# Optimization experiments

Measured on AMD Instinct MI355X. Metric: run time of the kernel, lower is better.

The kernel has to match this reference:

```python
import jax, jax.numpy as jnp
import numpy as np

B, S, HID, NH = 2, 2048, 1024, 16
HD = HID // NH  # head_dim = 64


def setup_inputs() -> dict:
    key = jax.random.key(0)
    ks = jax.random.split(key, 9)
    init = 0.02
    return {
        "x": jax.random.normal(ks[0], (B, S, HID), dtype=jnp.float32),
        "Wq": jax.random.normal(ks[1], (HID, HID), dtype=jnp.float32) * init,
        "bq": jnp.zeros((HID,), dtype=jnp.float32),
        "Wk": jax.random.normal(ks[2], (HID, HID), dtype=jnp.float32) * init,
        "bk": jnp.zeros((HID,), dtype=jnp.float32),
        "Wv": jax.random.normal(ks[3], (HID, HID), dtype=jnp.float32) * init,
        "bv": jnp.zeros((HID,), dtype=jnp.float32),
        "Wo": jax.random.normal(ks[4], (HID, HID), dtype=jnp.float32) * init,
        "bo": jnp.zeros((HID,), dtype=jnp.float32),
    }


def _split_heads(t):
    # [B, S, HID] -> [B, NH, S, HD]
    return t.reshape(B, S, NH, HD).transpose(0, 2, 1, 3)


def reference(x, Wq, bq, Wk, bk, Wv, bv, Wo, bo):
    q = _split_heads(x @ Wq.T + bq)
    k = _split_heads(x @ Wk.T + bk)
    v = _split_heads(x @ Wv.T + bv)

    # Faithful to source: scores = QK^T / (head_dim ** -0.5) == QK^T * sqrt(head_dim)
    inv_scale = jnp.asarray(HD ** (-0.5), dtype=x.dtype)
    scores = jnp.einsum("bhqd,bhkd->bhqk", q, k) / inv_scale

    causal_mask = jnp.triu(jnp.ones((S, S), dtype=bool), k=1)  # True above diagonal
    scores = jnp.where(causal_mask, jnp.asarray(-jnp.inf, dtype=scores.dtype), scores)
    attn = jax.nn.softmax(scores, axis=-1)  # dropout = identity (eval mode)

    ctx = jnp.einsum("bhqk,bhkd->bhqd", attn, v)
    ctx = ctx.transpose(0, 2, 1, 3).reshape(B, S, HID)
    out = ctx @ Wo.T + bo  # out_layer Linear; dropout = identity
    return out, attn
```

## Files before the change

kernel.cpp:

```cpp
#include <hip/hip_runtime.h>
#include <hip/hip_bf16.h>

#define BB   2
#define SS   2048
#define HID  1024
#define NH   16
#define HD   64
#define NEGS -30000.0f

typedef __bf16 bf16x8 __attribute__((ext_vector_type(8)));
typedef __bf16 bf16x4 __attribute__((ext_vector_type(4)));
typedef float  f32x4  __attribute__((ext_vector_type(4)));

static __device__ __forceinline__ f32x4 mfma_bf16(bf16x8 a, bf16x8 b, f32x4 c) {
    return __builtin_amdgcn_mfma_f32_16x16x32_bf16(a, b, c, 0, 0, 0);
}

static __device__ __forceinline__ void split_bf16(float f, __bf16* hp, __bf16* lp) {
    __bf16 h = (__bf16)f;
    *hp = h;
    *lp = (__bf16)(f - (float)h);
}

static __device__ __forceinline__ float clampf(float v, float lo, float hi) {
    return fminf(fmaxf(v, lo), hi);
}

static __device__ __forceinline__ void gll16(const __bf16* g, __bf16* l) {
    __builtin_amdgcn_global_load_lds((const void*)g, (void*)l, 16, 0, 0);
}

static __device__ __forceinline__ void barrier_lds() {
    asm volatile("s_waitcnt lgkmcnt(0)" ::: "memory");
    __builtin_amdgcn_sched_barrier(0);
    __builtin_amdgcn_s_barrier();
    __builtin_amdgcn_sched_barrier(0);
}

__global__ __launch_bounds__(256) void split_kernel(
    const float* __restrict__ x,
    const float* __restrict__ Wq, const float* __restrict__ Wk,
    const float* __restrict__ Wv, const float* __restrict__ Wo,
    __bf16* __restrict__ xh, __bf16* __restrict__ xl,
    __bf16* __restrict__ wqh, __bf16* __restrict__ wql,
    __bf16* __restrict__ wkh, __bf16* __restrict__ wkl,
    __bf16* __restrict__ wvh, __bf16* __restrict__ woh)
{
    const int which = blockIdx.y;
    const int i4 = blockIdx.x * 256 + threadIdx.x;
    if (which == 0) {
        const float4 v = ((const float4*)x)[i4];
        const float* p = (const float*)&v;
        bf16x4 h4, l4v;
#pragma unroll
        for (int j = 0; j < 4; j++) { __bf16 hh, ll; split_bf16(p[j], &hh, &ll); h4[j] = hh; l4v[j] = ll; }
        *(bf16x4*)&xh[(size_t)i4 * 4] = h4;
        *(bf16x4*)&xl[(size_t)i4 * 4] = l4v;
        return;
    }
    if (i4 >= (HID * HID) / 4) return;
    const float* src = which == 1 ? Wq : which == 2 ? Wk : which == 3 ? Wv : Wo;
    const float sc = (which == 1) ? 8.0f : 1.0f;
    const float4 v = ((const float4*)src)[i4];
    const float* p = (const float*)&v;
    bf16x4 h4, l4v;
#pragma unroll
    for (int j = 0; j < 4; j++) { __bf16 hh, ll; split_bf16(p[j] * sc, &hh, &ll); h4[j] = hh; l4v[j] = ll; }
    if (which == 1)      { *(bf16x4*)&wqh[(size_t)i4 * 4] = h4; *(bf16x4*)&wql[(size_t)i4 * 4] = l4v; }
    else if (which == 2) { *(bf16x4*)&wkh[(size_t)i4 * 4] = h4; *(bf16x4*)&wkl[(size_t)i4 * 4] = l4v; }
    else if (which == 3) { *(bf16x4*)&wvh[(size_t)i4 * 4] = h4; }
    else                 { *(bf16x4*)&woh[(size_t)i4 * 4] = h4; }
}

__global__ __launch_bounds__(256) void qkv_kernel(
    const __bf16* __restrict__ xh, const __bf16* __restrict__ xl,
    const __bf16* __restrict__ wqh, const __bf16* __restrict__ wql,
    const __bf16* __restrict__ wkh, const __bf16* __restrict__ wkl,
    const __bf16* __restrict__ wvh,
    const float* __restrict__ bq, const float* __restrict__ bk, const float* __restrict__ bv,
    __bf16* __restrict__ qh, __bf16* __restrict__ ql,
    __bf16* __restrict__ kh, __bf16* __restrict__ kl,
    __bf16* __restrict__ vt)
{
    __shared__ __align__(16) __bf16 smem[18432];
    __bf16* const Ah = smem;
    __bf16* const Al = smem + 4096;
    __bf16* const Bh = smem + 8192;
    __bf16* const Bl = smem + 12288;

    const int stream = blockIdx.x >> 3, ct = blockIdx.x & 7;
    const int t0 = blockIdx.y * 128, c0 = ct * 128;
    const bool qk = stream < 2;
    const __bf16* const Bhg = stream == 0 ? wqh : stream == 1 ? wkh : wvh;
    const __bf16* const Blg = stream == 0 ? wql : wkl;
    const float* const bias = stream == 0 ? bq : stream == 1 ? bk : bv;
    const float bscale = stream == 0 ? 8.0f : 1.0f;

    const int tid = threadIdx.x, wave = tid >> 6, lane = tid & 63;
    const int l16 = lane & 15, quad = lane >> 4;
    const int wr = wave >> 1, wc = wave & 1;

    const int ar0 = tid >> 2,         as0 = (tid & 3) ^ (ar0 & 3);
    const int ar1 = (256 + tid) >> 2, as1 = ((256 + tid) & 3) ^ (ar1 & 3);
    const size_t aoff0 = (size_t)(t0 + ar0) * HID + as0 * 8;
    const size_t aoff1 = (size_t)(t0 + ar1) * HID + as1 * 8;
    const size_t boff0 = (size_t)(c0 + ar0) * HID + as0 * 8;
    const size_t boff1 = (size_t)(c0 + ar1) * HID + as1 * 8;
    const int ld0 = wave << 9, ld1 = (4 + wave) << 9;

    const f32x4 zero4 = {0.f, 0.f, 0.f, 0.f};
    f32x4 acc[4][4];
#pragma unroll
    for (int i = 0; i < 4; i++)
#pragma unroll
        for (int j = 0; j < 4; j++) acc[i][j] = zero4;

    for (int k0 = 0; k0 < HID; k0 += 32) {
        __syncthreads();
        gll16(xh + aoff0 + k0, Ah + ld0);
        gll16(xh + aoff1 + k0, Ah + ld1);
        gll16(Bhg + boff0 + k0, Bh + ld0);
        gll16(Bhg + boff1 + k0, Bh + ld1);
        if (qk) {
            gll16(xl + aoff0 + k0, Al + ld0);
            gll16(xl + aoff1 + k0, Al + ld1);
            gll16(Blg + boff0 + k0, Bl + ld0);
            gll16(Blg + boff1 + k0, Bl + ld1);
        }
        __syncthreads();

        bf16x8 aH[4], aL[4], bHf[4], bLf[4];
#pragma unroll
        for (int mf = 0; mf < 4; mf++) {
            const int row = wr * 64 + mf * 16 + l16;
            const int off = row * 32 + ((quad ^ (row & 3)) << 3);
            aH[mf] = *(const bf16x8*)(Ah + off);
            if (qk) aL[mf] = *(const bf16x8*)(Al + off);
        }
#pragma unroll
        for (int nf = 0; nf < 4; nf++) {
            const int row = wc * 64 + nf * 16 + l16;
            const int off = row * 32 + ((quad ^ (row & 3)) << 3);
            bHf[nf] = *(const bf16x8*)(Bh + off);
            if (qk) bLf[nf] = *(const bf16x8*)(Bl + off);
        }
#pragma unroll
        for (int mf = 0; mf < 4; mf++)
#pragma unroll
            for (int nf = 0; nf < 4; nf++) {
                acc[mf][nf] = mfma_bf16(aH[mf], bHf[nf], acc[mf][nf]);
                if (qk) {
                    acc[mf][nf] = mfma_bf16(aH[mf], bLf[nf], acc[mf][nf]);
                    acc[mf][nf] = mfma_bf16(aL[mf], bHf[nf], acc[mf][nf]);
                }
            }
    }

    const int bidx = t0 >> 11;
    const int s0 = t0 & (SS - 1);

    if (qk) {
        __bf16* const hi = stream == 0 ? qh : kh;
        __bf16* const lo = stream == 0 ? ql : kl;
#pragma unroll
        for (int nf = 0; nf < 4; nf++) {
            const int dcol = c0 + wc * 64 + nf * 16 + l16;
            const int hh = dcol >> 6, d = dcol & 63;
            const float bv_ = bias[dcol] * bscale;
            const size_t ob = (size_t)(bidx * NH + hh) * SS * HD + d;
#pragma unroll
            for (int mf = 0; mf < 4; mf++)
#pragma unroll
                for (int r = 0; r < 4; r++) {
                    const int srow = s0 + wr * 64 + mf * 16 + quad * 4 + r;
                    const float v = clampf(acc[mf][nf][r] + bv_, -1e4f, 1e4f);
                    __bf16 hv, lv;
                    split_bf16(v, &hv, &lv);
                    hi[ob + (size_t)srow * HD] = hv;
                    lo[ob + (size_t)srow * HD] = lv;
                }
        }
    } else {
        __syncthreads();
        __bf16* const Vts = smem + wave * 4608;
#pragma unroll
        for (int nf = 0; nf < 4; nf++) {
            const int dloc = nf * 16 + l16;
            const float bv_ = bias[c0 + wc * 64 + dloc];
#pragma unroll
            for (int mf = 0; mf < 4; mf++)
#pragma unroll
                for (int r = 0; r < 4; r++)
                    Vts[dloc * 72 + mf * 16 + quad * 4 + r] =
                        (__bf16)clampf(acc[mf][nf][r] + bv_, -1e4f, 1e4f);
        }
        const int hh = (c0 + wc * 64) >> 6;
        const size_t vb = (size_t)(bidx * NH + hh) * HD * SS;
        const int sc0 = s0 + wr * 64;
#pragma unroll
        for (int j = 0; j < 8; j++) {
            const int idx = j * 64 + lane;
            const int d = idx >> 3, c8 = idx & 7;
            *(uint4*)&vt[vb + (size_t)d * SS + sc0 + c8 * 8] =
                *(const uint4*)&Vts[d * 72 + c8 * 8];
        }
    }
}

__global__ __launch_bounds__(256) void attn_kernel(
    const __bf16* __restrict__ qh, const __bf16* __restrict__ ql,
    const __bf16* __restrict__ kh, const __bf16* __restrict__ kl,
    const __bf16* __restrict__ vt,
    float* __restrict__ attn, __bf16* __restrict__ ctx)
{
    __shared__ __align__(16) __bf16 Qhs[64][72], Qls[64][72], Ps[64][72];
    __shared__ __align__(16) __bf16 Kh0[4096], Kl0[4096], Kh1[4096], Kl1[4096];
    __shared__ __align__(16) __bf16 Vt0[4096], Vt1[4096];

    const int bid = blockIdx.x;
    const int bh  = bid >> 5;
    const int qt  = 31 - (bid & 31);
    const int b   = bh >> 4, h = bh & 15;

    const int tid  = threadIdx.x;
    const int wave = tid >> 6, lane = tid & 63;
    const int l16  = lane & 15, quad = lane >> 4;

    const int sr0 = tid >> 3,         ss0 = (tid & 7) ^ (sr0 & 7);
    const int sr1 = (256 + tid) >> 3, ss1 = ((256 + tid) & 7) ^ (sr1 & 7);
    const size_t kq0 = (size_t)sr0 * HD + ss0 * 8;
    const size_t kq1 = (size_t)sr1 * HD + ss1 * 8;
    const size_t vq0 = (size_t)sr0 * SS + ss0 * 8;
    const size_t vq1 = (size_t)sr1 * SS + ss1 * 8;
    const int ld0 = wave << 9, ld1 = (4 + wave) << 9;

    const __bf16* const khp = kh + (size_t)bh * SS * HD;
    const __bf16* const klp = kl + (size_t)bh * SS * HD;
    const __bf16* const vtp = vt + (size_t)bh * HD * SS;

#define STAGE_K(kt_, KH, KL) do {                                   \
        const __bf16* kg_ = khp + (size_t)(kt_) * (64 * HD);        \
        const __bf16* lg_ = klp + (size_t)(kt_) * (64 * HD);        \
        gll16(kg_ + kq0, (KH) + ld0); gll16(kg_ + kq1, (KH) + ld1); \
        gll16(lg_ + kq0, (KL) + ld0); gll16(lg_ + kq1, (KL) + ld1); \
    } while (0)
#define STAGE_V(kt_, VT) do {                                       \
        const __bf16* vg_ = vtp + (size_t)(kt_) * 64;               \
        gll16(vg_ + vq0, (VT) + ld0); gll16(vg_ + vq1, (VT) + ld1); \
    } while (0)

    {
        const size_t base = ((size_t)bh * SS + qt * 64) * HD;
#pragma unroll
        for (int i = 0; i < 2; i++) {
            const int idx = tid + i * 256;
            const int row = idx >> 3, c8 = idx & 7;
            *(uint4*)&Qhs[row][c8 * 8] = *(const uint4*)&qh[base + row * HD + c8 * 8];
            *(uint4*)&Qls[row][c8 * 8] = *(const uint4*)&ql[base + row * HD + c8 * 8];
        }
    }
    STAGE_K(0, Kh0, Kl0);
    __syncthreads();

    bf16x8 aHq[2], aLq[2];
#pragma unroll
    for (int ks = 0; ks < 2; ks++) {
        aHq[ks] = *(const bf16x8*)&Qhs[wave * 16 + l16][ks * 32 + quad * 8];
        aLq[ks] = *(const bf16x8*)&Qls[wave * 16 + l16][ks * 32 + quad * 8];
    }

    float m4[4], l4[4];
#pragma unroll
    for (int r = 0; r < 4; r++) { m4[r] = NEGS; l4[r] = 0.f; }
    const f32x4 zero4 = {0.f, 0.f, 0.f, 0.f};

    for (int kt = 0; kt <= qt; kt++) {
        if (kt) __syncthreads();
        if (kt < qt) {
            if (kt & 1) STAGE_K(kt + 1, Kh0, Kl0);
            else        STAGE_K(kt + 1, Kh1, Kl1);
        }
        const __bf16* const Khc = (kt & 1) ? Kh1 : Kh0;
        const __bf16* const Klc = (kt & 1) ? Kl1 : Kl0;

        f32x4 sacc[4] = {zero4, zero4, zero4, zero4};
#pragma unroll
        for (int ks = 0; ks < 2; ks++)
#pragma unroll
            for (int c = 0; c < 4; c++) {
                const int krow = c * 16 + l16;
                const int ko = krow * 64 + (((ks * 4 + quad) ^ (krow & 7)) << 3);
                const bf16x8 bH = *(const bf16x8*)(Khc + ko);
                const bf16x8 bL = *(const bf16x8*)(Klc + ko);
                sacc[c] = mfma_bf16(aHq[ks], bH, sacc[c]);
                sacc[c] = mfma_bf16(aHq[ks], bL, sacc[c]);
                sacc[c] = mfma_bf16(aLq[ks], bH, sacc[c]);
            }
        if (kt == qt) {
#pragma unroll
            for (int c = 0; c < 4; c++) {
                const int col = c * 16 + l16;
#pragma unroll
                for (int r = 0; r < 4; r++)
                    if (col > wave * 16 + quad * 4 + r) sacc[c][r] = NEGS;
            }
        }
#pragma unroll
        for (int r = 0; r < 4; r++) {
            const float mx = fmaxf(fmaxf(sacc[0][r], sacc[1][r]),
                                   fmaxf(sacc[2][r], sacc[3][r]));
            const float mn = fmaxf(m4[r], mx);
            l4[r] = l4[r] * __expf(m4[r] - mn)
                  + __expf(sacc[0][r] - mn) + __expf(sacc[1][r] - mn)
                  + __expf(sacc[2][r] - mn) + __expf(sacc[3][r] - mn);
            m4[r] = mn;
        }
    }

    float il[4];
#pragma unroll
    for (int r = 0; r < 4; r++) {
#pragma unroll
        for (int off = 1; off < 16; off <<= 1) {
            const float mo  = __shfl_xor(m4[r], off);
            const float lo_ = __shfl_xor(l4[r], off);
            const float mn  = fmaxf(m4[r], mo);
            l4[r] = l4[r] * __expf(m4[r] - mn) + lo_ * __expf(mo - mn);
            m4[r] = mn;
        }
        il[r] = (l4[r] > 0.f) ? (1.0f / l4[r]) : 0.f;
    }

    f32x4 cacc[4] = {zero4, zero4, zero4, zero4};

    __syncthreads();
    STAGE_K(0, Kh0, Kl0);
    STAGE_V(0, Vt0);

    for (int kt = 0; kt <= qt; kt++) {
        __syncthreads();
        if (kt < qt) {
            if (kt & 1) { STAGE_K(kt + 1, Kh0, Kl0); STAGE_V(kt + 1, Vt0); }
            else        { STAGE_K(kt + 1, Kh1, Kl1); STAGE_V(kt + 1, Vt1); }
        }
        const __bf16* const Khc = (kt & 1) ? Kh1 : Kh0;
        const __bf16* const Klc = (kt & 1) ? Kl1 : Kl0;
        const __bf16* const Vtc = (kt & 1) ? Vt1 : Vt0;

        f32x4 sacc[4] = {zero4, zero4, zero4, zero4};
#pragma unroll
        for (int ks = 0; ks < 2; ks++)
#pragma unroll
            for (int c = 0; c < 4; c++) {
                const int krow = c * 16 + l16;
                const int ko = krow * 64 + (((ks * 4 + quad) ^ (krow & 7)) << 3);
                const bf16x8 bH = *(const bf16x8*)(Khc + ko);
                const bf16x8 bL = *(const bf16x8*)(Klc + ko);
                sacc[c] = mfma_bf16(aHq[ks], bH, sacc[c]);
                sacc[c] = mfma_bf16(aHq[ks], bL, sacc[c]);
                sacc[c] = mfma_bf16(aLq[ks], bH, sacc[c]);
            }
        if (kt == qt) {
#pragma unroll
            for (int c = 0; c < 4; c++) {
                const int col = c * 16 + l16;
#pragma unroll
                for (int r = 0; r < 4; r++)
                    if (col > wave * 16 + quad * 4 + r) sacc[c][r] = NEGS;
            }
        }
#pragma unroll
        for (int c = 0; c < 4; c++)
#pragma unroll
            for (int r = 0; r < 4; r++) {
                const float p = clampf(__expf(sacc[c][r] - m4[r]) * il[r], 0.f, 1.f);
                Ps[wave * 16 + quad * 4 + r][c * 16 + l16] = (__bf16)p;
            }
        barrier_lds();

#pragma unroll
        for (int i = 0; i < 2; i++) {
            const int idx = tid + i * 256;
            const int row = idx >> 3, c8 = idx & 7;
            const size_t o = ((size_t)bh * SS + qt * 64 + row) * SS + kt * 64 + c8 * 8;
            __bf16 tmp[8];
            *(uint4*)tmp = *(const uint4*)&Ps[row][c8 * 8];
            float4 f0, f1;
            f0.x = (float)tmp[0]; f0.y = (float)tmp[1];
            f0.z = (float)tmp[2]; f0.w = (float)tmp[3];
            f1.x = (float)tmp[4]; f1.y = (float)tmp[5];
            f1.z = (float)tmp[6]; f1.w = (float)tmp[7];
            *(float4*)&attn[o]     = f0;
            *(float4*)&attn[o + 4] = f1;
        }
#pragma unroll
        for (int ks = 0; ks < 2; ks++) {
            const bf16x8 ap = *(const bf16x8*)&Ps[wave * 16 + l16][ks * 32 + quad * 8];
#pragma unroll
            for (int dt = 0; dt < 4; dt++) {
                const int vrow = dt * 16 + l16;
                const int vo = vrow * 64 + (((ks * 4 + quad) ^ (vrow & 7)) << 3);
                cacc[dt] = mfma_bf16(ap, *(const bf16x8*)(Vtc + vo), cacc[dt]);
            }
        }
    }

    const float4 zf4 = {0.f, 0.f, 0.f, 0.f};
    for (int kt = qt + 1; kt < SS / 64; kt++) {
#pragma unroll
        for (int i = 0; i < 4; i++) {
            const int idx = tid + i * 256;
            const int row = idx >> 4, c4 = idx & 15;
            const size_t o = ((size_t)bh * SS + qt * 64 + row) * SS + kt * 64 + c4 * 4;
            *(float4*)&attn[o] = zf4;
        }
    }

#pragma unroll
    for (int dt = 0; dt < 4; dt++) {
        const int d = dt * 16 + l16;
#pragma unroll
        for (int r = 0; r < 4; r++) {
            const int srow = qt * 64 + wave * 16 + quad * 4 + r;
            ctx[(size_t)(b * SS + srow) * HID + h * 64 + d] =
                (__bf16)clampf(cacc[dt][r], -1e4f, 1e4f);
        }
    }
#undef STAGE_K
#undef STAGE_V
}

__global__ __launch_bounds__(256) void out_kernel(
    const __bf16* __restrict__ ctx, const __bf16* __restrict__ woh,
    const float* __restrict__ bo, float* __restrict__ out)
{
    __shared__ __align__(16) __bf16 As[4096], Bs[4096];

    const int o0 = blockIdx.x * 128;
    const int t0 = blockIdx.y * 128;

    const int tid = threadIdx.x, wave = tid >> 6, lane = tid & 63;
    const int l16 = lane & 15, quad = lane >> 4;
    const int wr = wave >> 1, wc = wave & 1;

    const int ar0 = tid >> 2,         as0 = (tid & 3) ^ (ar0 & 3);
    const int ar1 = (256 + tid) >> 2, as1 = ((256 + tid) & 3) ^ (ar1 & 3);
    const size_t aoff0 = (size_t)(t0 + ar0) * HID + as0 * 8;
    const size_t aoff1 = (size_t)(t0 + ar1) * HID + as1 * 8;
    const size_t boff0 = (size_t)(o0 + ar0) * HID + as0 * 8;
    const size_t boff1 = (size_t)(o0 + ar1) * HID + as1 * 8;
    const int ld0 = wave << 9, ld1 = (4 + wave) << 9;

    const f32x4 zero4 = {0.f, 0.f, 0.f, 0.f};
    f32x4 acc[4][4];
#pragma unroll
    for (int i = 0; i < 4; i++)
#pragma unroll
        for (int j = 0; j < 4; j++) acc[i][j] = zero4;

    for (int k0 = 0; k0 < HID; k0 += 32) {
        __syncthreads();
        gll16(ctx + aoff0 + k0, As + ld0);
        gll16(ctx + aoff1 + k0, As + ld1);
        gll16(woh + boff0 + k0, Bs + ld0);
        gll16(woh + boff1 + k0, Bs + ld1);
        __syncthreads();

        bf16x8 aH[4], bHf[4];
#pragma unroll
        for (int mf = 0; mf < 4; mf++) {
            const int row = wr * 64 + mf * 16 + l16;
            aH[mf] = *(const bf16x8*)(As + row * 32 + ((quad ^ (row & 3)) << 3));
        }
#pragma unroll
        for (int nf = 0; nf < 4; nf++) {
            const int row = wc * 64 + nf * 16 + l16;
            bHf[nf] = *(const bf16x8*)(Bs + row * 32 + ((quad ^ (row & 3)) << 3));
        }
#pragma unroll
        for (int mf = 0; mf < 4; mf++)
#pragma unroll
            for (int nf = 0; nf < 4; nf++)
                acc[mf][nf] = mfma_bf16(aH[mf], bHf[nf], acc[mf][nf]);
    }

#pragma unroll
    for (int nf = 0; nf < 4; nf++) {
        const int dcol = o0 + wc * 64 + nf * 16 + l16;
        const float bias = bo[dcol];
#pragma unroll
        for (int mf = 0; mf < 4; mf++)
#pragma unroll
            for (int r = 0; r < 4; r++) {
                const int t = t0 + wr * 64 + mf * 16 + quad * 4 + r;
                out[(size_t)t * HID + dcol] = clampf(acc[mf][nf][r] + bias, -1e4f, 1e4f);
            }
    }
}

extern "C" void kernel_launch(void* const* d_in, const int* in_sizes, int n_in,
                              void* d_out, int out_size, void* d_ws, size_t ws_size,
                              hipStream_t stream) {
    const float* x  = (const float*)d_in[0];
    const float* Wq = (const float*)d_in[1];
    const float* bq = (const float*)d_in[2];
    const float* Wk = (const float*)d_in[3];
    const float* bk = (const float*)d_in[4];
    const float* Wv = (const float*)d_in[5];
    const float* bv = (const float*)d_in[6];
    const float* Wo = (const float*)d_in[7];
    const float* bo = (const float*)d_in[8];

    float* out  = (float*)d_out;
    float* attn = out + (size_t)BB * SS * HID;

    const size_t NQ = (size_t)BB * NH * SS * HD;
    const size_t NW = (size_t)HID * HID;
    __bf16* ws  = (__bf16*)d_ws;
    __bf16* qh  = ws;
    __bf16* ql  = ws + NQ;
    __bf16* kh  = ws + 2 * NQ;
    __bf16* kl  = ws + 3 * NQ;
    __bf16* vt  = ws + 4 * NQ;
    __bf16* xh  = ws + 5 * NQ;
    __bf16* xl  = ws + 6 * NQ;
    __bf16* wqh = ws + 7 * NQ;
    __bf16* wql = wqh + NW;
    __bf16* wkh = wqh + 2 * NW;
    __bf16* wkl = wqh + 3 * NW;
    __bf16* wvh = wqh + 4 * NW;
    __bf16* woh = wqh + 5 * NW;
    __bf16* ctx = xh;

    split_kernel<<<dim3(4096, 5), 256, 0, stream>>>(x, Wq, Wk, Wv, Wo,
                                                    xh, xl, wqh, wql, wkh, wkl, wvh, woh);
    qkv_kernel<<<dim3(24, 32), 256, 0, stream>>>(xh, xl, wqh, wql, wkh, wkl, wvh,
                                                 bq, bk, bv, qh, ql, kh, kl, vt);
    attn_kernel<<<dim3(1024), 256, 0, stream>>>(qh, ql, kh, kl, vt, attn, ctx);
    out_kernel<<<dim3(8, 32), 256, 0, stream>>>(ctx, woh, bo, out);
}
```

Baseline: 817.8 us.

## Restructure attention into 128-row tiles with paired causal segments and staged stores

The attention kernel now uses 512-thread blocks over 128-query-row tiles. Each block processes two paired tiles (qt and 15-qt) so causal work is balanced across 256 blocks, and blocks are mapped so consecutive ones share the same head for K/V reuse. Q is loaded straight into registers, ctx is staged through LDS for coalesced 16-byte stores, and a dummy LDS pad is added to cap occupancy. The QKV epilogue also stages hi/lo tiles through shared memory so global writes are vectorised instead of scalar. The tradeoffs are fewer blocks in flight and extra LDS passes with barriers.

```diff
diff --git a/kernel.cpp b/kernel.cpp
--- a/kernel.cpp
+++ b/kernel.cpp
@@ -160,25 +160,38 @@
     const int s0 = t0 & (SS - 1);
 
     if (qk) {
-        __bf16* const hi = stream == 0 ? qh : kh;
-        __bf16* const lo = stream == 0 ? ql : kl;
-#pragma unroll
-        for (int nf = 0; nf < 4; nf++) {
-            const int dcol = c0 + wc * 64 + nf * 16 + l16;
-            const int hh = dcol >> 6, d = dcol & 63;
-            const float bv_ = bias[dcol] * bscale;
-            const size_t ob = (size_t)(bidx * NH + hh) * SS * HD + d;
-#pragma unroll
-            for (int mf = 0; mf < 4; mf++)
-#pragma unroll
-                for (int r = 0; r < 4; r++) {
-                    const int srow = s0 + wr * 64 + mf * 16 + quad * 4 + r;
-                    const float v = clampf(acc[mf][nf][r] + bv_, -1e4f, 1e4f);
-                    __bf16 hv, lv;
-                    split_bf16(v, &hv, &lv);
-                    hi[ob + (size_t)srow * HD] = hv;
-                    lo[ob + (size_t)srow * HD] = lv;
-                }
+        __bf16* const Es = smem;
+        __bf16* const hi_arr = stream == 0 ? qh : kh;
+        __bf16* const lo_arr = stream == 0 ? ql : kl;
+#pragma unroll
+        for (int pass = 0; pass < 2; pass++) {
+            __syncthreads();
+#pragma unroll
+            for (int nf = 0; nf < 4; nf++) {
+                const int dcl = wc * 64 + nf * 16 + l16;
+                const float bv_ = bias[c0 + dcl] * bscale;
+#pragma unroll
+                for (int mf = 0; mf < 4; mf++)
+#pragma unroll
+                    for (int r = 0; r < 4; r++) {
+                        const int srl = wr * 64 + mf * 16 + quad * 4 + r;
+                        const float v = clampf(acc[mf][nf][r] + bv_, -1e4f, 1e4f);
+                        __bf16 hv, lv;
+                        split_bf16(v, &hv, &lv);
+                        Es[srl * 132 + dcl] = pass ? lv : hv;
+                    }
+            }
+            __syncthreads();
+            __bf16* const dst = pass ? lo_arr : hi_arr;
+#pragma unroll
+            for (int i = 0; i < 8; i++) {
+                const int idx = tid + i * 256;
+                const int row = idx >> 4, c16 = idx & 15;
+                const int hh = (c0 >> 6) + (c16 >> 3);
+                const int dd = (c16 & 7) * 8;
+                const size_t o = ((size_t)(bidx * NH + hh) * SS + (s0 + row)) * HD + dd;
+                *(uint4*)&dst[o] = *(const uint4*)&Es[row * 132 + c16 * 8];
+            }
         }
     } else {
         __syncthreads();
@@ -207,225 +220,235 @@
     }
 }
 
-__global__ __launch_bounds__(256) void attn_kernel(
+__global__ __launch_bounds__(512) void attn_kernel(
     const __bf16* __restrict__ qh, const __bf16* __restrict__ ql,
     const __bf16* __restrict__ kh, const __bf16* __restrict__ kl,
     const __bf16* __restrict__ vt,
     float* __restrict__ attn, __bf16* __restrict__ ctx)
 {
-    __shared__ __align__(16) __bf16 Qhs[64][72], Qls[64][72], Ps[64][72];
     __shared__ __align__(16) __bf16 Kh0[4096], Kl0[4096], Kh1[4096], Kl1[4096];
     __shared__ __align__(16) __bf16 Vt0[4096], Vt1[4096];
+    __shared__ __align__(16) __bf16 Ps[128][72];
+    __shared__ __align__(16) __bf16 _occ_pad[8192];
 
     const int bid = blockIdx.x;
-    const int bh  = bid >> 5;
-    const int qt  = 31 - (bid & 31);
+    const int g   = bid & 7;
+    const int ii  = bid >> 3;
+    const int bh  = g + 8 * (ii & 3);
+    const int p   = ii >> 2;
     const int b   = bh >> 4, h = bh & 15;
 
     const int tid  = threadIdx.x;
     const int wave = tid >> 6, lane = tid & 63;
     const int l16  = lane & 15, quad = lane >> 4;
 
-    const int sr0 = tid >> 3,         ss0 = (tid & 7) ^ (sr0 & 7);
-    const int sr1 = (256 + tid) >> 3, ss1 = ((256 + tid) & 7) ^ (sr1 & 7);
-    const size_t kq0 = (size_t)sr0 * HD + ss0 * 8;
-    const size_t kq1 = (size_t)sr1 * HD + ss1 * 8;
-    const size_t vq0 = (size_t)sr0 * SS + ss0 * 8;
-    const size_t vq1 = (size_t)sr1 * SS + ss1 * 8;
-    const int ld0 = wave << 9, ld1 = (4 + wave) << 9;
+    const int sr = tid >> 3, ssw = (tid & 7) ^ (sr & 7);
+    const size_t kq = (size_t)sr * HD + ssw * 8;
+    const size_t vq = (size_t)sr * SS + ssw * 8;
+    const int ldw = wave << 9;
 
     const __bf16* const khp = kh + (size_t)bh * SS * HD;
     const __bf16* const klp = kl + (size_t)bh * SS * HD;
     const __bf16* const vtp = vt + (size_t)bh * HD * SS;
 
-#define STAGE_K(kt_, KH, KL) do {                                   \
-        const __bf16* kg_ = khp + (size_t)(kt_) * (64 * HD);        \
-        const __bf16* lg_ = klp + (size_t)(kt_) * (64 * HD);        \
-        gll16(kg_ + kq0, (KH) + ld0); gll16(kg_ + kq1, (KH) + ld1); \
-        gll16(lg_ + kq0, (KL) + ld0); gll16(lg_ + kq1, (KL) + ld1); \
+#define STAGE_K(j_, KH, KL) do {                                  \
+        const __bf16* kg_ = khp + (size_t)(j_) * (64 * HD);       \
+        const __bf16* lg_ = klp + (size_t)(j_) * (64 * HD);       \
+        gll16(kg_ + kq, (KH) + ldw); gll16(lg_ + kq, (KL) + ldw); \
     } while (0)
-#define STAGE_V(kt_, VT) do {                                       \
-        const __bf16* vg_ = vtp + (size_t)(kt_) * 64;               \
-        gll16(vg_ + vq0, (VT) + ld0); gll16(vg_ + vq1, (VT) + ld1); \
+#define STAGE_V(j_, VT) do {                                      \
+        const __bf16* vg_ = vtp + (size_t)(j_) * 64;              \
+        gll16(vg_ + vq, (VT) + ldw);                              \
     } while (0)
 
-    {
-        const size_t base = ((size_t)bh * SS + qt * 64) * HD;
+    const f32x4 zero4 = {0.f, 0.f, 0.f, 0.f};
+
+    for (int seg = 0; seg < 2; seg++) {
+        const int qt = seg ? p : (15 - p);
+        const int nj = 2 * qt + 2;
+
+        bf16x8 aHq[2], aLq[2];
+        {
+            const size_t qrow = ((size_t)bh * SS + qt * 128 + wave * 16 + l16) * HD;
+#pragma unroll
+            for (int ks = 0; ks < 2; ks++) {
+                aHq[ks] = *(const bf16x8*)&qh[qrow + ks * 32 + quad * 8];
+                aLq[ks] = *(const bf16x8*)&ql[qrow + ks * 32 + quad * 8];
+            }
+        }
+
+        float m4[4], l4[4];
+#pragma unroll
+        for (int r = 0; r < 4; r++) { m4[r] = NEGS; l4[r] = 0.f; }
+
+        __syncthreads();
+        STAGE_K(0, Kh0, Kl0);
+        __syncthreads();
+
+        for (int j = 0; j < nj; j++) {
+            if (j) __syncthreads();
+            if (j < nj - 1) {
+                if (j & 1) STAGE_K(j + 1, Kh0, Kl0);
+                else       STAGE_K(j + 1, Kh1, Kl1);
+            }
+            const __bf16* const Khc = (j & 1) ? Kh1 : Kh0;
+            const __bf16* const Klc = (j & 1) ? Kl1 : Kl0;
+
+            f32x4 sacc[4] = {zero4, zero4, zero4, zero4};
+#pragma unroll
+            for (int ks = 0; ks < 2; ks++)
+#pragma unroll
+                for (int c = 0; c < 4; c++) {
+                    const int krow = c * 16 + l16;
+                    const int ko = krow * 64 + (((ks * 4 + quad) ^ (krow & 7)) << 3);
+                    const bf16x8 bH = *(const bf16x8*)(Khc + ko);
+                    const bf16x8 bL = *(const bf16x8*)(Klc + ko);
+                    sacc[c] = mfma_bf16(aHq[ks], bH, sacc[c]);
+                    sacc[c] = mfma_bf16(aHq[ks], bL, sacc[c]);
+                    sacc[c] = mfma_bf16(aLq[ks], bH, sacc[c]);
+                }
+            if (j >= 2 * qt) {
+                const int cb = j * 64, qr = qt * 128 + wave * 16 + quad * 4;
+#pragma unroll
+                for (int c = 0; c < 4; c++) {
+                    const int col = cb + c * 16 + l16;
+#pragma unroll
+                    for (int r = 0; r < 4; r++)
+                        if (col > qr + r) sacc[c][r] = NEGS;
+                }
+            }
+#pragma unroll
+            for (int r = 0; r < 4; r++) {
+                const float mx = fmaxf(fmaxf(sacc[0][r], sacc[1][r]),
+                                       fmaxf(sacc[2][r], sacc[3][r]));
+                const float mn = fmaxf(m4[r], mx);
+                l4[r] = l4[r] * __expf(m4[r] - mn)
+                      + __expf(sacc[0][r] - mn) + __expf(sacc[1][r] - mn)
+                      + __expf(sacc[2][r] - mn) + __expf(sacc[3][r] - mn);
+                m4[r] = mn;
+            }
+        }
+
+        float il[4];
+#pragma unroll
+        for (int r = 0; r < 4; r++) {
+#pragma unroll
+            for (int off = 1; off < 16; off <<= 1) {
+                const float mo  = __shfl_xor(m4[r], off);
+                const float lo_ = __shfl_xor(l4[r], off);
+                const float mn  = fmaxf(m4[r], mo);
+                l4[r] = l4[r] * __expf(m4[r] - mn) + lo_ * __expf(mo - mn);
+                m4[r] = mn;
+            }
+            il[r] = (l4[r] > 0.f) ? (1.0f / l4[r]) : 0.f;
+        }
+
+        f32x4 cacc[4] = {zero4, zero4, zero4, zero4};
+
+        __syncthreads();
+        STAGE_K(0, Kh0, Kl0);
+        STAGE_V(0, Vt0);
+
+        for (int j = 0; j < nj; j++) {
+            __syncthreads();
+            if (j < nj - 1) {
+                if (j & 1) { STAGE_K(j + 1, Kh0, Kl0); STAGE_V(j + 1, Vt0); }
+                else       { STAGE_K(j + 1, Kh1, Kl1); STAGE_V(j + 1, Vt1); }
+            }
+            const __bf16* const Khc = (j & 1) ? Kh1 : Kh0;
+            const __bf16* const Klc = (j & 1) ? Kl1 : Kl0;
+            const __bf16* const Vtc = (j & 1) ? Vt1 : Vt0;
+
+            f32x4 sacc[4] = {zero4, zero4, zero4, zero4};
+#pragma unroll
+            for (int ks = 0; ks < 2; ks++)
+#pragma unroll
+                for (int c = 0; c < 4; c++) {
+                    const int krow = c * 16 + l16;
+                    const int ko = krow * 64 + (((ks * 4 + quad) ^ (krow & 7)) << 3);
+                    const bf16x8 bH = *(const bf16x8*)(Khc + ko);
+                    const bf16x8 bL = *(const bf16x8*)(Klc + ko);
+                    sacc[c] = mfma_bf16(aHq[ks], bH, sacc[c]);
+                    sacc[c] = mfma_bf16(aHq[ks], bL, sacc[c]);
+                    sacc[c] = mfma_bf16(aLq[ks], bH, sacc[c]);
+                }
+            if (j >= 2 * qt) {
+                const int cb = j * 64, qr = qt * 128 + wave * 16 + quad * 4;
+#pragma unroll
+                for (int c = 0; c < 4; c++) {
+                    const int col = cb + c * 16 + l16;
+#pragma unroll
+                    for (int r = 0; r < 4; r++)
+                        if (col > qr + r) sacc[c][r] = NEGS;
+                }
+            }
+#pragma unroll
+            for (int c = 0; c < 4; c++)
+#pragma unroll
+                for (int r = 0; r < 4; r++) {
+                    const float pv = clampf(__expf(sacc[c][r] - m4[r]) * il[r], 0.f, 1.f);
+                    Ps[wave * 16 + quad * 4 + r][c * 16 + l16] = (__bf16)pv;
+                }
+            barrier_lds();
+
+#pragma unroll
+            for (int i = 0; i < 2; i++) {
+                const int idx = tid + i * 512;
+                const int row = idx >> 3, c8 = idx & 7;
+                const size_t o = ((size_t)bh * SS + qt * 128 + row) * SS + j * 64 + c8 * 8;
+                __bf16 tmp[8];
+                *(uint4*)tmp = *(const uint4*)&Ps[row][c8 * 8];
+                float4 f0, f1;
+                f0.x = (float)tmp[0]; f0.y = (float)tmp[1];
+                f0.z = (float)tmp[2]; f0.w = (float)tmp[3];
+                f1.x = (float)tmp[4]; f1.y = (float)tmp[5];
+                f1.z = (float)tmp[6]; f1.w = (float)tmp[7];
+                *(float4*)&attn[o]     = f0;
+                *(float4*)&attn[o + 4] = f1;
+            }
+#pragma unroll
+            for (int ks = 0; ks < 2; ks++) {
+                const bf16x8 ap = *(const bf16x8*)&Ps[wave * 16 + l16][ks * 32 + quad * 8];
+#pragma unroll
+                for (int dt = 0; dt < 4; dt++) {
+                    const int vrow = dt * 16 + l16;
+                    const int vo = vrow * 64 + (((ks * 4 + quad) ^ (vrow & 7)) << 3);
+                    cacc[dt] = mfma_bf16(ap, *(const bf16x8*)(Vtc + vo), cacc[dt]);
+                }
+            }
+        }
+
+        const float4 zf4 = {0.f, 0.f, 0.f, 0.f};
+        for (int j = nj; j < SS / 64; j++) {
+#pragma unroll
+            for (int i = 0; i < 4; i++) {
+                const int idx = tid + i * 512;
+                const int row = idx >> 4, c4 = idx & 15;
+                const size_t o = ((size_t)bh * SS + qt * 128 + row) * SS + j * 64 + c4 * 4;
+                *(float4*)&attn[o] = zf4;
+            }
+        }
+
+        __syncthreads();
+#pragma unroll
+        for (int dt = 0; dt < 4; dt++) {
+            const int d = dt * 16 + l16;
+#pragma unroll
+            for (int r = 0; r < 4; r++)
+                Ps[wave * 16 + quad * 4 + r][d] =
+                    (__bf16)clampf(cacc[dt][r], -1e4f, 1e4f);
+        }
+        __syncthreads();
 #pragma unroll
         for (int i = 0; i < 2; i++) {
-            const int idx = tid + i * 256;
+            const int idx = tid + i * 512;
             const int row = idx >> 3, c8 = idx & 7;
-            *(uint4*)&Qhs[row][c8 * 8] = *(const uint4*)&qh[base + row * HD + c8 * 8];
-            *(uint4*)&Qls[row][c8 * 8] = *(const uint4*)&ql[base + row * HD + c8 * 8];
+            *(uint4*)&ctx[(size_t)(b * SS + qt * 128 + row) * HID + h * 64 + c8 * 8] =
+                *(const uint4*)&Ps[row][c8 * 8];
         }
     }
-    STAGE_K(0, Kh0, Kl0);
-    __syncthreads();
-
-    bf16x8 aHq[2], aLq[2];
-#pragma unroll
-    for (int ks = 0; ks < 2; ks++) {
-        aHq[ks] = *(const bf16x8*)&Qhs[wave * 16 + l16][ks * 32 + quad * 8];
-        aLq[ks] = *(const bf16x8*)&Qls[wave * 16 + l16][ks * 32 + quad * 8];
-    }
-
-    float m4[4], l4[4];
-#pragma unroll
-    for (int r = 0; r < 4; r++) { m4[r] = NEGS; l4[r] = 0.f; }
-    const f32x4 zero4 = {0.f, 0.f, 0.f, 0.f};
-
-    for (int kt = 0; kt <= qt; kt++) {
-        if (kt) __syncthreads();
-        if (kt < qt) {
-            if (kt & 1) STAGE_K(kt + 1, Kh0, Kl0);
-            else        STAGE_K(kt + 1, Kh1, Kl1);
-        }
-        const __bf16* const Khc = (kt & 1) ? Kh1 : Kh0;
-        const __bf16* const Klc = (kt & 1) ? Kl1 : Kl0;
-
-        f32x4 sacc[4] = {zero4, zero4, zero4, zero4};
-#pragma unroll
-        for (int ks = 0; ks < 2; ks++)
-#pragma unroll
-            for (int c = 0; c < 4; c++) {
-                const int krow = c * 16 + l16;
-                const int ko = krow * 64 + (((ks * 4 + quad) ^ (krow & 7)) << 3);
-                const bf16x8 bH = *(const bf16x8*)(Khc + ko);
-                const bf16x8 bL = *(const bf16x8*)(Klc + ko);
-                sacc[c] = mfma_bf16(aHq[ks], bH, sacc[c]);
-                sacc[c] = mfma_bf16(aHq[ks], bL, sacc[c]);
-                sacc[c] = mfma_bf16(aLq[ks], bH, sacc[c]);
-            }
-        if (kt == qt) {
-#pragma unroll
-            for (int c = 0; c < 4; c++) {
-                const int col = c * 16 + l16;
-#pragma unroll
-                for (int r = 0; r < 4; r++)
-                    if (col > wave * 16 + quad * 4 + r) sacc[c][r] = NEGS;
-            }
-        }
-#pragma unroll
-        for (int r = 0; r < 4; r++) {
-            const float mx = fmaxf(fmaxf(sacc[0][r], sacc[1][r]),
-                                   fmaxf(sacc[2][r], sacc[3][r]));
-            const float mn = fmaxf(m4[r], mx);
-            l4[r] = l4[r] * __expf(m4[r] - mn)
-                  + __expf(sacc[0][r] - mn) + __expf(sacc[1][r] - mn)
-                  + __expf(sacc[2][r] - mn) + __expf(sacc[3][r] - mn);
-            m4[r] = mn;
-        }
-    }
-
-    float il[4];
-#pragma unroll
-    for (int r = 0; r < 4; r++) {
-#pragma unroll
-        for (int off = 1; off < 16; off <<= 1) {
-            const float mo  = __shfl_xor(m4[r], off);
-            const float lo_ = __shfl_xor(l4[r], off);
-            const float mn  = fmaxf(m4[r], mo);
-            l4[r] = l4[r] * __expf(m4[r] - mn) + lo_ * __expf(mo - mn);
-            m4[r] = mn;
-        }
-        il[r] = (l4[r] > 0.f) ? (1.0f / l4[r]) : 0.f;
-    }
-
-    f32x4 cacc[4] = {zero4, zero4, zero4, zero4};
-
-    __syncthreads();
-    STAGE_K(0, Kh0, Kl0);
-    STAGE_V(0, Vt0);
-
-    for (int kt = 0; kt <= qt; kt++) {
-        __syncthreads();
-        if (kt < qt) {
-            if (kt & 1) { STAGE_K(kt + 1, Kh0, Kl0); STAGE_V(kt + 1, Vt0); }
-            else        { STAGE_K(kt + 1, Kh1, Kl1); STAGE_V(kt + 1, Vt1); }
-        }
-        const __bf16* const Khc = (kt & 1) ? Kh1 : Kh0;
-        const __bf16* const Klc = (kt & 1) ? Kl1 : Kl0;
-        const __bf16* const Vtc = (kt & 1) ? Vt1 : Vt0;
-
-        f32x4 sacc[4] = {zero4, zero4, zero4, zero4};
-#pragma unroll
-        for (int ks = 0; ks < 2; ks++)
-#pragma unroll
-            for (int c = 0; c < 4; c++) {
-                const int krow = c * 16 + l16;
-                const int ko = krow * 64 + (((ks * 4 + quad) ^ (krow & 7)) << 3);
-                const bf16x8 bH = *(const bf16x8*)(Khc + ko);
-                const bf16x8 bL = *(const bf16x8*)(Klc + ko);
-                sacc[c] = mfma_bf16(aHq[ks], bH, sacc[c]);
-                sacc[c] = mfma_bf16(aHq[ks], bL, sacc[c]);
-                sacc[c] = mfma_bf16(aLq[ks], bH, sacc[c]);
-            }
-        if (kt == qt) {
-#pragma unroll
-            for (int c = 0; c < 4; c++) {
-                const int col = c * 16 + l16;
-#pragma unroll
-                for (int r = 0; r < 4; r++)
-                    if (col > wave * 16 + quad * 4 + r) sacc[c][r] = NEGS;
-            }
-        }
-#pragma unroll
-        for (int c = 0; c < 4; c++)
-#pragma unroll
-            for (int r = 0; r < 4; r++) {
-                const float p = clampf(__expf(sacc[c][r] - m4[r]) * il[r], 0.f, 1.f);
-                Ps[wave * 16 + quad * 4 + r][c * 16 + l16] = (__bf16)p;
-            }
-        barrier_lds();
-
-#pragma unroll
-        for (int i = 0; i < 2; i++) {
-            const int idx = tid + i * 256;
-            const int row = idx >> 3, c8 = idx & 7;
-            const size_t o = ((size_t)bh * SS + qt * 64 + row) * SS + kt * 64 + c8 * 8;
-            __bf16 tmp[8];
-            *(uint4*)tmp = *(const uint4*)&Ps[row][c8 * 8];
-            float4 f0, f1;
-            f0.x = (float)tmp[0]; f0.y = (float)tmp[1];
-            f0.z = (float)tmp[2]; f0.w = (float)tmp[3];
-            f1.x = (float)tmp[4]; f1.y = (float)tmp[5];
-            f1.z = (float)tmp[6]; f1.w = (float)tmp[7];
-            *(float4*)&attn[o]     = f0;
-            *(float4*)&attn[o + 4] = f1;
-        }
-#pragma unroll
-        for (int ks = 0; ks < 2; ks++) {
-            const bf16x8 ap = *(const bf16x8*)&Ps[wave * 16 + l16][ks * 32 + quad * 8];
-#pragma unroll
-            for (int dt = 0; dt < 4; dt++) {
-                const int vrow = dt * 16 + l16;
-                const int vo = vrow * 64 + (((ks * 4 + quad) ^ (vrow & 7)) << 3);
-                cacc[dt] = mfma_bf16(ap, *(const bf16x8*)(Vtc + vo), cacc[dt]);
-            }
-        }
-    }
-
-    const float4 zf4 = {0.f, 0.f, 0.f, 0.f};
-    for (int kt = qt + 1; kt < SS / 64; kt++) {
-#pragma unroll
-        for (int i = 0; i < 4; i++) {
-            const int idx = tid + i * 256;
-            const int row = idx >> 4, c4 = idx & 15;
-            const size_t o = ((size_t)bh * SS + qt * 64 + row) * SS + kt * 64 + c4 * 4;
-            *(float4*)&attn[o] = zf4;
-        }
-    }
-
-#pragma unroll
-    for (int dt = 0; dt < 4; dt++) {
-        const int d = dt * 16 + l16;
-#pragma unroll
-        for (int r = 0; r < 4; r++) {
-            const int srow = qt * 64 + wave * 16 + quad * 4 + r;
-            ctx[(size_t)(b * SS + srow) * HID + h * 64 + d] =
-                (__bf16)clampf(cacc[dt][r], -1e4f, 1e4f);
-        }
-    }
+
+    if ((int)blockIdx.x < 0) ((volatile __bf16*)_occ_pad)[0] = Ps[0][0];
 #undef STAGE_K
 #undef STAGE_V
 }
@@ -536,6 +559,6 @@
                                                     xh, xl, wqh, wql, wkh, wkl, wvh, woh);
     qkv_kernel<<<dim3(24, 32), 256, 0, stream>>>(xh, xl, wqh, wql, wkh, wkl, wvh,
                                                  bq, bk, bv, qh, ql, kh, kl, vt);
-    attn_kernel<<<dim3(1024), 256, 0, stream>>>(qh, ql, kh, kl, vt, attn, ctx);
+    attn_kernel<<<dim3(256), 512, 0, stream>>>(qh, ql, kh, kl, vt, attn, ctx);
     out_kernel<<<dim3(8, 32), 256, 0, stream>>>(ctx, woh, bo, out);
 }
```

Result: faster. 765.8 us (-6.4%).
